# Performance work log

Measured on AMD Instinct MI355X. Metric: run time of the kernel, lower is better.

## Reference

```python
import jax, jax.numpy as jnp
import numpy as np

VOCAB = 8192
DIM = 64
COMMITMENT = 0.25
N = 65536


def setup_inputs() -> dict:
    key = jax.random.key(0)
    kx, ke = jax.random.split(key)
    x = jax.random.normal(kx, (N, DIM), dtype=jnp.float32)
    # matches nn.Embedding weight init uniform_(-0.5, 0.5)
    emb_weight = jax.random.uniform(ke, (VOCAB, DIM), dtype=jnp.float32, minval=-0.5, maxval=0.5)
    return {"x": x, "emb_weight": emb_weight}


def reference(x, emb_weight):
    # cdist(x, E, p=2): squared form gives identical argmin (sqrt is monotone)
    x2 = jnp.sum(x * x, axis=-1, keepdims=True)            # [N, 1]
    e2 = jnp.sum(emb_weight * emb_weight, axis=-1)         # [V]
    d2 = x2 + e2[None, :] - 2.0 * (x @ emb_weight.T)       # [N, V]
    idx = jnp.argmin(d2, axis=-1)                          # [N] int

    quantised = emb_weight[idx]                            # [N, D] gather

    codebook_loss = jnp.mean((quantised - jax.lax.stop_gradient(x)) ** 2)
    e_latent_loss = jnp.mean((jax.lax.stop_gradient(quantised) - x) ** 2)
    loss = codebook_loss + COMMITMENT * e_latent_loss

    # straight-through estimator
    quantised_ste = x + jax.lax.stop_gradient(quantised - x)
    return quantised_ste, loss, idx
```

## Files before the change

kernel.cpp:

```cpp
#include <hip/hip_runtime.h>

#define N 65536
#define D 64
#define V 8192
#define LOSS_OFF (N * D)
#define IDX_OFF (N * D + 1)
#define MARGIN 0.02f
#define NPART 4

typedef _Float16 half8 __attribute__((ext_vector_type(8)));
typedef float f32x4 __attribute__((ext_vector_type(4)));

typedef __attribute__((address_space(1))) const void gas_t;
typedef __attribute__((address_space(3))) void las_t;

#define DOT16(s, A0, A1, A2, A3, B0, B1, B2, B3)                         \
    s = fmaf(A0.x, B0.x, s); s = fmaf(A0.y, B0.y, s);                    \
    s = fmaf(A0.z, B0.z, s); s = fmaf(A0.w, B0.w, s);                    \
    s = fmaf(A1.x, B1.x, s); s = fmaf(A1.y, B1.y, s);                    \
    s = fmaf(A1.z, B1.z, s); s = fmaf(A1.w, B1.w, s);                    \
    s = fmaf(A2.x, B2.x, s); s = fmaf(A2.y, B2.y, s);                    \
    s = fmaf(A2.z, B2.z, s); s = fmaf(A2.w, B2.w, s);                    \
    s = fmaf(A3.x, B3.x, s); s = fmaf(A3.y, B3.y, s);                    \
    s = fmaf(A3.z, B3.z, s); s = fmaf(A3.w, B3.w, s);

__device__ __forceinline__ unsigned enc32(float f) {
    unsigned u = __float_as_uint(f);
    return (u & 0x80000000u) ? ~u : (u | 0x80000000u);
}

__global__ __launch_bounds__(256) void k_split(const float* __restrict__ E,
                                               _Float16* __restrict__ Ef16,
                                               float* __restrict__ e2,
                                               float* __restrict__ dout,
                                               int* __restrict__ fcount) {
    const int t = blockIdx.x * 256 + threadIdx.x;
    if (t == 0) {
        dout[LOSS_OFF] = 0.0f;
        *fcount = 0;
    }
    const int row = t >> 3;
    const int seg = t & 7;
    const float4* p = (const float4*)(E + (size_t)row * D + seg * 8);
    float4 a = p[0], b = p[1];
    float s = a.x * a.x + a.y * a.y + a.z * a.z + a.w * a.w +
              b.x * b.x + b.y * b.y + b.z * b.z + b.w * b.w;
    s += __shfl_xor(s, 1, 8);
    s += __shfl_xor(s, 2, 8);
    s += __shfl_xor(s, 4, 8);
    if (seg == 0) e2[row] = s;
    half8 h;
    h[0] = (_Float16)(-2.0f * a.x); h[1] = (_Float16)(-2.0f * a.y);
    h[2] = (_Float16)(-2.0f * a.z); h[3] = (_Float16)(-2.0f * a.w);
    h[4] = (_Float16)(-2.0f * b.x); h[5] = (_Float16)(-2.0f * b.y);
    h[6] = (_Float16)(-2.0f * b.z); h[7] = (_Float16)(-2.0f * b.w);
    *(half8*)(Ef16 + (size_t)row * D + seg * 8) = h;
}

#define MERGE(M1, M2, GID, L, PID)          \
    {                                       \
        bool bt = (L) < (M1);               \
        float m2c = bt ? (M1) : (L);        \
        (M2) = fminf((M2), m2c);            \
        (GID) = bt ? (PID) : (GID);         \
        (M1) = fminf((M1), (L));            \
    }

__global__ __launch_bounds__(512) void k_argmin(const float* __restrict__ X,
                                                const _Float16* __restrict__ Ef16,
                                                const float* __restrict__ e2,
                                                float4* __restrict__ part4) {
    __shared__ __align__(16) _Float16 els[2][8192];

    const int tid = threadIdx.x;
    const int lane = tid & 63;
    const int wave = tid >> 6;
    const int P = blockIdx.x & 3;
    const int rb = blockIdx.x >> 2;
    const int c4 = lane & 15;
    const int kg = lane >> 4;
    const int wrow = rb * 256 + wave * 32;
    const int sw = c4 & 7;
    const int k0off = (kg ^ sw) * 8;
    const int k1off = ((4 + kg) ^ sw) * 8;
    const int ch0 = P * 16;

    half8 x00, x01, x10, x11;
    {
        const float* xr0 = X + (size_t)(wrow + c4) * D;
        const float* xr1 = X + (size_t)(wrow + 16 + c4) * D;
#pragma unroll
        for (int f = 0; f < 2; ++f) {
            float4 lo = *(const float4*)(xr0 + f * 32 + kg * 8);
            float4 hi = *(const float4*)(xr0 + f * 32 + kg * 8 + 4);
            half8 h;
            h[0] = (_Float16)lo.x; h[1] = (_Float16)lo.y;
            h[2] = (_Float16)lo.z; h[3] = (_Float16)lo.w;
            h[4] = (_Float16)hi.x; h[5] = (_Float16)hi.y;
            h[6] = (_Float16)hi.z; h[7] = (_Float16)hi.w;
            if (f == 0) x00 = h; else x01 = h;
        }
#pragma unroll
        for (int f = 0; f < 2; ++f) {
            float4 lo = *(const float4*)(xr1 + f * 32 + kg * 8);
            float4 hi = *(const float4*)(xr1 + f * 32 + kg * 8 + 4);
            half8 h;
            h[0] = (_Float16)lo.x; h[1] = (_Float16)lo.y;
            h[2] = (_Float16)lo.z; h[3] = (_Float16)lo.w;
            h[4] = (_Float16)hi.x; h[5] = (_Float16)hi.y;
            h[6] = (_Float16)hi.z; h[7] = (_Float16)hi.w;
            if (f == 0) x10 = h; else x11 = h;
        }
    }

    const int q0 = tid, q1 = tid + 512;
    const _Float16* gs0 = Ef16 + (size_t)(ch0 * 128 + (q0 >> 3)) * 64 + ((q0 & 7) ^ ((q0 >> 3) & 7)) * 8;
    const _Float16* gs1 = Ef16 + (size_t)(ch0 * 128 + (q1 >> 3)) * 64 + ((q1 & 7) ^ ((q1 >> 3) & 7)) * 8;
    const int ld0 = q0 * 8, ld1 = q1 * 8;

#define STAGE(BUF)                                                            \
    {                                                                         \
        __builtin_amdgcn_global_load_lds((gas_t*)gs0, (las_t*)&els[BUF][ld0], 16, 0, 0); \
        __builtin_amdgcn_global_load_lds((gas_t*)gs1, (las_t*)&els[BUF][ld1], 16, 0, 0); \
        gs0 += 8192; gs1 += 8192;                                             \
    }

    float m1a = 3.4e38f, m2a = 3.4e38f, m1b = 3.4e38f, m2b = 3.4e38f;
    unsigned gida = 0, gidb = 0;

#define TSTEP(T, E2Q)                                                         \
    {                                                                         \
        const half8 a0 = *(const half8*)&els[buf][(T * 16 + c4) * 64 + k0off];\
        const half8 a1 = *(const half8*)&els[buf][(T * 16 + c4) * 64 + k1off];\
        f32x4 acc0 = __builtin_amdgcn_mfma_f32_16x16x32_f16(a0, x00, E2Q, 0, 0, 0); \
        acc0 = __builtin_amdgcn_mfma_f32_16x16x32_f16(a1, x01, acc0, 0, 0, 0);\
        f32x4 acc1 = __builtin_amdgcn_mfma_f32_16x16x32_f16(a0, x10, E2Q, 0, 0, 0); \
        acc1 = __builtin_amdgcn_mfma_f32_16x16x32_f16(a1, x11, acc1, 0, 0, 0);\
        float Lq0 = fminf(fminf(acc0[0], acc0[1]), fminf(acc0[2], acc0[3]));  \
        float Lq1 = fminf(fminf(acc1[0], acc1[1]), fminf(acc1[2], acc1[3]));  \
        const unsigned pid = pidq + T * 4;                                    \
        MERGE(m1a, m2a, gida, Lq0, pid)                                       \
        MERGE(m1b, m2b, gidb, Lq1, pid)                                       \
    }

    STAGE(0)
    const f32x4* e2p = (const f32x4*)(e2 + (size_t)ch0 * 128) + kg;
    unsigned pidq = (unsigned)(ch0 * 32 + kg);

    for (int ci = 0; ci < 16; ++ci) {
        __syncthreads();
        const f32x4 e2q0 = e2p[0],  e2q1 = e2p[4],  e2q2 = e2p[8],  e2q3 = e2p[12];
        const f32x4 e2q4 = e2p[16], e2q5 = e2p[20], e2q6 = e2p[24], e2q7 = e2p[28];
        e2p += 32;
        if (ci < 15) STAGE((ci + 1) & 1)
        const int buf = ci & 1;

        TSTEP(0, e2q0) TSTEP(1, e2q1) TSTEP(2, e2q2) TSTEP(3, e2q3)
        TSTEP(4, e2q4) TSTEP(5, e2q5) TSTEP(6, e2q6) TSTEP(7, e2q7)
        pidq += 32;
    }

#pragma unroll
    for (int off = 16; off < 64; off <<= 1) {
        float o1, o2;
        unsigned og;
        o1 = __shfl_xor(m1a, off, 64); o2 = __shfl_xor(m2a, off, 64);
        og = (unsigned)__shfl_xor((int)gida, off, 64);
        m2a = fminf(fminf(fmaxf(m1a, o1), m2a), o2);
        if (o1 < m1a) gida = og;
        m1a = fminf(m1a, o1);
        o1 = __shfl_xor(m1b, off, 64); o2 = __shfl_xor(m2b, off, 64);
        og = (unsigned)__shfl_xor((int)gidb, off, 64);
        m2b = fminf(fminf(fmaxf(m1b, o1), m2b), o2);
        if (o1 < m1b) gidb = og;
        m1b = fminf(m1b, o1);
    }

    if (lane < 16) {
        float4 r;
        r.x = m1a; r.y = m2a; r.z = __uint_as_float(gida); r.w = 0.0f;
        part4[(size_t)P * N + wrow + lane] = r;
        r.x = m1b; r.y = m2b; r.z = __uint_as_float(gidb);
        part4[(size_t)P * N + wrow + 16 + lane] = r;
    }
}

__global__ __launch_bounds__(256) void k_group(const float* __restrict__ X,
                                               const float* __restrict__ E,
                                               const float* __restrict__ e2,
                                               const float4* __restrict__ part4,
                                               int* __restrict__ fcount,
                                               int* __restrict__ flist,
                                               unsigned long long* __restrict__ packed,
                                               float* __restrict__ lpart,
                                               float* __restrict__ dout) {
    const int lane = threadIdx.x & 63;
    const int wave = threadIdx.x >> 6;
    const int lig = lane & 15;
    const int grp = lane >> 4;
    const int row = blockIdx.x * 16 + wave * 4 + grp;

    float m1, m2;
    unsigned g;
    {
        const float4 r0 = part4[row];
        m1 = r0.x; m2 = r0.y; g = __float_as_uint(r0.z);
#pragma unroll
        for (int k = 1; k < NPART; ++k) {
            const float4 r = part4[(size_t)k * N + row];
            const unsigned rg = __float_as_uint(r.z);
            if (r.x < m1) {
                m2 = fminf(m2, m1);
                m1 = r.x;
                g = rg;
            } else {
                m2 = fminf(m2, r.x);
            }
            m2 = fminf(m2, r.y);
        }
    }

    float lossp = 0.0f;
    if (m2 - m1 < MARGIN) {
        if (lig == 0) {
            int p = atomicAdd(fcount, 1);
            flist[p] = row;
            packed[p] = ~0ull;
        }
    } else {
        const int e = lig >> 2;
        const int dg = lig & 3;
        const int v = (int)(g << 2) + e;
        const float4* xp = (const float4*)(X + (size_t)row * D) + dg * 4;
        float4 xa0 = xp[0], xa1 = xp[1], xa2 = xp[2], xa3 = xp[3];
        const float4* ep = (const float4*)(E + (size_t)v * D) + dg * 4;
        float4 b0 = ep[0], b1 = ep[1], b2 = ep[2], b3 = ep[3];
        float s = 0.0f;
        DOT16(s, xa0, xa1, xa2, xa3, b0, b1, b2, b3)
        s += __shfl_xor(s, 1, 64);
        s += __shfl_xor(s, 2, 64);
        float d = fmaf(-2.0f, s, e2[v]);
        int bidx = v;
#pragma unroll
        for (int off = 4; off < 16; off <<= 1) {
            float ob = __shfl_xor(d, off, 64);
            int oi = __shfl_xor(bidx, off, 64);
            if (ob < d || (ob == d && oi < bidx)) { d = ob; bidx = oi; }
        }
        if (lig == 0) dout[IDX_OFF + row] = (float)bidx;
        float4 x4 = *(const float4*)(X + (size_t)row * D + lig * 4);
        float4 q4 = *(const float4*)(E + (size_t)bidx * D + lig * 4);
        float4 o;
        o.x = x4.x + (q4.x - x4.x);
        o.y = x4.y + (q4.y - x4.y);
        o.z = x4.z + (q4.z - x4.z);
        o.w = x4.w + (q4.w - x4.w);
        *(float4*)(dout + (size_t)row * D + lig * 4) = o;
        float dx = q4.x - x4.x, dy = q4.y - x4.y, dz = q4.z - x4.z,
              dw = q4.w - x4.w;
        lossp = dx * dx + dy * dy + dz * dz + dw * dw;
    }

#pragma unroll
    for (int off = 32; off; off >>= 1) lossp += __shfl_down(lossp, off, 64);
    __shared__ float ps[4];
    if (lane == 0) ps[wave] = lossp;
    __syncthreads();
    if (threadIdx.x == 0) lpart[blockIdx.x] = ps[0] + ps[1] + ps[2] + ps[3];
}

__global__ __launch_bounds__(256) void k_full(const float* __restrict__ X,
                                              const float* __restrict__ E,
                                              const float* __restrict__ e2,
                                              const int* __restrict__ fcount,
                                              const int* __restrict__ flist,
                                              unsigned long long* __restrict__ packed) {
    const int nf = *fcount;
    if (nf == 0) return;
    const int nq = (nf + 3) >> 2;
    const int total = nq * 8;
    const int lane = threadIdx.x & 63;
    const int nwaves = gridDim.x * 4;
    int item = blockIdx.x * 4 + (threadIdx.x >> 6);
    const int e4 = lane >> 2;
    const int dg = lane & 3;

    for (; item < total; item += nwaves) {
        const int qi = item >> 3;
        const int c = item & 7;
        const int f0 = qi * 4;
        const int f1 = min(f0 + 1, nf - 1);
        const int f2 = min(f0 + 2, nf - 1);
        const int f3 = min(f0 + 3, nf - 1);
        const int r0 = flist[f0], r1 = flist[f1], r2 = flist[f2], r3 = flist[f3];

        const float4* xp0 = (const float4*)(X + (size_t)r0 * D) + dg * 4;
        const float4* xp1 = (const float4*)(X + (size_t)r1 * D) + dg * 4;
        const float4* xp2 = (const float4*)(X + (size_t)r2 * D) + dg * 4;
        const float4* xp3 = (const float4*)(X + (size_t)r3 * D) + dg * 4;
        float4 xa0 = xp0[0], xa1 = xp0[1], xa2 = xp0[2], xa3 = xp0[3];
        float4 xb0 = xp1[0], xb1 = xp1[1], xb2 = xp1[2], xb3 = xp1[3];
        float4 xc0 = xp2[0], xc1 = xp2[1], xc2 = xp2[2], xc3 = xp2[3];
        float4 xd0 = xp3[0], xd1 = xp3[1], xd2 = xp3[2], xd3 = xp3[3];

        unsigned long long k0 = ~0ull, k1 = ~0ull, k2 = ~0ull, k3 = ~0ull;

#pragma unroll 2
        for (int it = 0; it < 64; ++it) {
            const int v = c * 1024 + it * 16 + e4;
            const float4* ep = (const float4*)(E + (size_t)v * D) + dg * 4;
            float4 b0 = ep[0], b1 = ep[1], b2 = ep[2], b3 = ep[3];
            float s0 = 0.0f, s1 = 0.0f, s2 = 0.0f, s3 = 0.0f;
            DOT16(s0, xa0, xa1, xa2, xa3, b0, b1, b2, b3)
            DOT16(s1, xb0, xb1, xb2, xb3, b0, b1, b2, b3)
            DOT16(s2, xc0, xc1, xc2, xc3, b0, b1, b2, b3)
            DOT16(s3, xd0, xd1, xd2, xd3, b0, b1, b2, b3)
            s0 += __shfl_xor(s0, 1, 64); s0 += __shfl_xor(s0, 2, 64);
            s1 += __shfl_xor(s1, 1, 64); s1 += __shfl_xor(s1, 2, 64);
            s2 += __shfl_xor(s2, 1, 64); s2 += __shfl_xor(s2, 2, 64);
            s3 += __shfl_xor(s3, 1, 64); s3 += __shfl_xor(s3, 2, 64);
            const float ev = e2[v];
            const unsigned long long vb = (unsigned long long)(unsigned)v;
            unsigned long long t;
            t = ((unsigned long long)enc32(fmaf(-2.0f, s0, ev)) << 32) | vb;
            k0 = t < k0 ? t : k0;
            t = ((unsigned long long)enc32(fmaf(-2.0f, s1, ev)) << 32) | vb;
            k1 = t < k1 ? t : k1;
            t = ((unsigned long long)enc32(fmaf(-2.0f, s2, ev)) << 32) | vb;
            k2 = t < k2 ? t : k2;
            t = ((unsigned long long)enc32(fmaf(-2.0f, s3, ev)) << 32) | vb;
            k3 = t < k3 ? t : k3;
        }

#pragma unroll
        for (int off = 4; off < 64; off <<= 1) {
            unsigned lo, hi;
            unsigned long long o;
            lo = __shfl_xor((unsigned)k0, off, 64); hi = __shfl_xor((unsigned)(k0 >> 32), off, 64);
            o = ((unsigned long long)hi << 32) | lo; k0 = o < k0 ? o : k0;
            lo = __shfl_xor((unsigned)k1, off, 64); hi = __shfl_xor((unsigned)(k1 >> 32), off, 64);
            o = ((unsigned long long)hi << 32) | lo; k1 = o < k1 ? o : k1;
            lo = __shfl_xor((unsigned)k2, off, 64); hi = __shfl_xor((unsigned)(k2 >> 32), off, 64);
            o = ((unsigned long long)hi << 32) | lo; k2 = o < k2 ? o : k2;
            lo = __shfl_xor((unsigned)k3, off, 64); hi = __shfl_xor((unsigned)(k3 >> 32), off, 64);
            o = ((unsigned long long)hi << 32) | lo; k3 = o < k3 ? o : k3;
        }

        if (lane == 0) {
            atomicMin(&packed[f0], k0);
            atomicMin(&packed[f1], k1);
            atomicMin(&packed[f2], k2);
            atomicMin(&packed[f3], k3);
        }
    }
}

__global__ __launch_bounds__(256) void k_out2(const float* __restrict__ X,
                                              const float* __restrict__ E,
                                              const int* __restrict__ fcount,
                                              const int* __restrict__ flist,
                                              const unsigned long long* __restrict__ packed,
                                              const float* __restrict__ lpart,
                                              float* __restrict__ dout) {
    const int lane = threadIdx.x & 63;
    const int wave = threadIdx.x >> 6;
    float lossp = 0.0f;
    if (wave == 0) lossp += lpart[blockIdx.x * 64 + lane];

    const int nf = *fcount;
    const int nwaves = gridDim.x * 4;
    for (int i = blockIdx.x * 4 + wave; i < nf; i += nwaves) {
        const int row = flist[i];
        const int idx = (int)(unsigned)(packed[i] & 0xffffffffull);
        if (lane == 0) dout[IDX_OFF + row] = (float)idx;
        if (lane < 16) {
            float4 x4 = *(const float4*)(X + (size_t)row * D + lane * 4);
            float4 q4 = *(const float4*)(E + (size_t)idx * D + lane * 4);
            float4 o;
            o.x = x4.x + (q4.x - x4.x);
            o.y = x4.y + (q4.y - x4.y);
            o.z = x4.z + (q4.z - x4.z);
            o.w = x4.w + (q4.w - x4.w);
            *(float4*)(dout + (size_t)row * D + lane * 4) = o;
            float dx = q4.x - x4.x, dy = q4.y - x4.y, dz = q4.z - x4.z,
                  dw = q4.w - x4.w;
            lossp += dx * dx + dy * dy + dz * dz + dw * dw;
        }
    }

#pragma unroll
    for (int off = 32; off; off >>= 1) lossp += __shfl_down(lossp, off, 64);
    __shared__ float ps[4];
    if (lane == 0) ps[wave] = lossp;
    __syncthreads();
    if (threadIdx.x == 0) {
        float tot = ps[0] + ps[1] + ps[2] + ps[3];
        atomicAdd(dout + LOSS_OFF, tot * (1.25f / ((float)N * (float)D)));
    }
}

extern "C" void kernel_launch(void* const* d_in, const int* in_sizes, int n_in,
                              void* d_out, int out_size, void* d_ws,
                              size_t ws_size, hipStream_t stream) {
    const float* X = (const float*)d_in[0];
    const float* E = (const float*)d_in[1];
    float* out = (float*)d_out;

    char* ws = (char*)d_ws;
    _Float16* Ef16 = (_Float16*)ws;
    float* e2 = (float*)(ws + 1048576);
    int* fcount = (int*)(ws + 1081344);
    int* flist = (int*)(ws + 1081600);
    unsigned long long* packed = (unsigned long long*)(ws + 1343744);
    float* lpart = (float*)(ws + 1868032);
    float4* part4 = (float4*)(ws + 1933568);

    k_split<<<256, 256, 0, stream>>>(E, Ef16, e2, out, fcount);
    k_argmin<<<(N / 256) * NPART, 512, 0, stream>>>(X, Ef16, e2, part4);
    k_group<<<N / 16, 256, 0, stream>>>(X, E, e2, part4, fcount, flist, packed, lpart, out);
    k_full<<<1024, 256, 0, stream>>>(X, E, e2, fcount, flist, packed);
    k_out2<<<64, 256, 0, stream>>>(X, E, fcount, flist, packed, lpart, out);
}
```

Baseline: 174.8 us.

## Coarsen argmin tracking to 16-code groups and widen exact rescore

The per-tile top-2 tracking in the MFMA loop now merges the running minimum over four tiles (groups of 16 codes) instead of after each tile, which removes most of the MERGE compare/select work in the hot loop. The exact fp32 rescoring stage then has to evaluate 16 candidate codes per row (four passes of four codes per lane) instead of four. The group-id mapping to code indices is rebuilt to match. The trade is fewer hot-loop instructions for more global loads and dot products in the refinement phase, and a coarser margin check that may send more rows to the fallback path.

```diff
diff --git a/kernel.cpp b/kernel.cpp
--- a/kernel.cpp
+++ b/kernel.cpp
@@ -136,16 +136,13 @@
         acc0 = __builtin_amdgcn_mfma_f32_16x16x32_f16(a1, x01, acc0, 0, 0, 0);\
         f32x4 acc1 = __builtin_amdgcn_mfma_f32_16x16x32_f16(a0, x10, E2Q, 0, 0, 0); \
         acc1 = __builtin_amdgcn_mfma_f32_16x16x32_f16(a1, x11, acc1, 0, 0, 0);\
-        float Lq0 = fminf(fminf(acc0[0], acc0[1]), fminf(acc0[2], acc0[3]));  \
-        float Lq1 = fminf(fminf(acc1[0], acc1[1]), fminf(acc1[2], acc1[3]));  \
-        const unsigned pid = pidq + T * 4;                                    \
-        MERGE(m1a, m2a, gida, Lq0, pid)                                       \
-        MERGE(m1b, m2b, gidb, Lq1, pid)                                       \
+        La = fminf(fminf(fminf(fminf(La, acc0[0]), acc0[1]), acc0[2]), acc0[3]); \
+        Lb = fminf(fminf(fminf(fminf(Lb, acc1[0]), acc1[1]), acc1[2]), acc1[3]); \
     }
 
     STAGE(0)
     const f32x4* e2p = (const f32x4*)(e2 + (size_t)ch0 * 128) + kg;
-    unsigned pidq = (unsigned)(ch0 * 32 + kg);
+    unsigned pidb = (unsigned)(ch0 * 8 + kg);
 
     for (int ci = 0; ci < 16; ++ci) {
         __syncthreads();
@@ -155,9 +152,15 @@
         if (ci < 15) STAGE((ci + 1) & 1)
         const int buf = ci & 1;
 
+        float La = 3.4e38f, Lb = 3.4e38f;
         TSTEP(0, e2q0) TSTEP(1, e2q1) TSTEP(2, e2q2) TSTEP(3, e2q3)
+        MERGE(m1a, m2a, gida, La, pidb)
+        MERGE(m1b, m2b, gidb, Lb, pidb)
+        La = 3.4e38f; Lb = 3.4e38f;
         TSTEP(4, e2q4) TSTEP(5, e2q5) TSTEP(6, e2q6) TSTEP(7, e2q7)
-        pidq += 32;
+        MERGE(m1a, m2a, gida, La, pidb + 4)
+        MERGE(m1b, m2b, gidb, Lb, pidb + 4)
+        pidb += 8;
     }
 
 #pragma unroll
@@ -228,24 +231,32 @@
             packed[p] = ~0ull;
         }
     } else {
-        const int e = lig >> 2;
+        const int es = lig >> 2;
         const int dg = lig & 3;
-        const int v = (int)(g << 2) + e;
+        const int base = (int)((g >> 3) * 128 + ((g >> 2) & 1) * 64 +
+                               (g & 3) * 4 + es);
         const float4* xp = (const float4*)(X + (size_t)row * D) + dg * 4;
         float4 xa0 = xp[0], xa1 = xp[1], xa2 = xp[2], xa3 = xp[3];
-        const float4* ep = (const float4*)(E + (size_t)v * D) + dg * 4;
-        float4 b0 = ep[0], b1 = ep[1], b2 = ep[2], b3 = ep[3];
-        float s = 0.0f;
-        DOT16(s, xa0, xa1, xa2, xa3, b0, b1, b2, b3)
-        s += __shfl_xor(s, 1, 64);
-        s += __shfl_xor(s, 2, 64);
-        float d = fmaf(-2.0f, s, e2[v]);
-        int bidx = v;
+
+        float best = 3.4e38f;
+        int bidx = 0x7fffffff;
+#pragma unroll
+        for (int eg = 0; eg < 4; ++eg) {
+            const int v = base + eg * 16;
+            const float4* ep = (const float4*)(E + (size_t)v * D) + dg * 4;
+            float4 b0 = ep[0], b1 = ep[1], b2 = ep[2], b3 = ep[3];
+            float s = 0.0f;
+            DOT16(s, xa0, xa1, xa2, xa3, b0, b1, b2, b3)
+            s += __shfl_xor(s, 1, 64);
+            s += __shfl_xor(s, 2, 64);
+            float d = fmaf(-2.0f, s, e2[v]);
+            if (d < best) { best = d; bidx = v; }
+        }
 #pragma unroll
         for (int off = 4; off < 16; off <<= 1) {
-            float ob = __shfl_xor(d, off, 64);
+            float ob = __shfl_xor(best, off, 64);
             int oi = __shfl_xor(bidx, off, 64);
-            if (ob < d || (ob == d && oi < bidx)) { d = ob; bidx = oi; }
+            if (ob < best || (ob == best && oi < bidx)) { best = ob; bidx = oi; }
         }
         if (lig == 0) dout[IDX_OFF + row] = (float)bidx;
         float4 x4 = *(const float4*)(X + (size_t)row * D + lig * 4);
```

Measured after the change: 182.1 us. +4.2%, slower.
